# Performance work log

Measured on AMD Instinct MI355X. Metric: run time of the kernel, lower is better.

The kernel has to match this reference:

```python
import jax, jax.numpy as jnp
import numpy as np

S, B, I, H = 512, 128, 256, 512  # seq_len, batch, input_size, hidden_size


def setup_inputs() -> dict:
    key = jax.random.key(0)
    ks = jax.random.split(key, 5)
    # Gates stacked in order (f, i, o, c), each Linear init'd like nn.Linear
    lim_w = 1.0 / np.sqrt(I)
    lim_u = 1.0 / np.sqrt(H)
    x = jax.random.normal(ks[0], (S, B, I), dtype=jnp.float32)
    W = jax.random.uniform(ks[1], (4 * H, I), minval=-lim_w, maxval=lim_w, dtype=jnp.float32)
    bW = jax.random.uniform(ks[2], (4 * H,), minval=-lim_w, maxval=lim_w, dtype=jnp.float32)
    U = jax.random.uniform(ks[3], (4 * H, H), minval=-lim_u, maxval=lim_u, dtype=jnp.float32)
    bU = jax.random.uniform(ks[4], (4 * H,), minval=-lim_u, maxval=lim_u, dtype=jnp.float32)
    return {"x": x, "W": W, "bW": bW, "U": U, "bU": bU}


def reference(x, W, bW, U, bU):
    """LSTM over time-major x. Gates stacked (f, i, o, c) along dim 0 of W/U.
    Returns (h_seq [S,B,H], h_final [B,H], c_final [B,H]).
    The original's bf/bi/bo/bc buffers are zeros and thus omitted."""
    Hh = U.shape[1]
    # Input projection for all timesteps + both Linear biases, done once.
    xg = jnp.einsum('sbi,gi->sbg', x, W) + bW + bU  # [S, B, 4H]

    def step(carry, xg_t):
        h, c = carry
        g = xg_t + h @ U.T  # [B, 4H]
        f = jax.nn.sigmoid(g[:, 0 * Hh:1 * Hh])
        i = jax.nn.sigmoid(g[:, 1 * Hh:2 * Hh])
        o = jax.nn.sigmoid(g[:, 2 * Hh:3 * Hh])
        cand = jnp.tanh(g[:, 3 * Hh:4 * Hh])
        c_new = f * c + i * cand
        h_new = o * jnp.tanh(c_new)
        return (h_new, c_new), h_new

    b = x.shape[1]
    init = (jnp.zeros((b, Hh), x.dtype), jnp.zeros((b, Hh), x.dtype))
    (h_fin, c_fin), h_seq = jax.lax.scan(step, init, xg)
    return h_seq, h_fin, c_fin
```

## Files before the change

### kernel.cpp

```cpp
#include <hip/hip_runtime.h>
#include <hip/hip_bf16.h>


#define S_LEN 512
#define BATCH 128
#define ISZ   256
#define HSZ   512

typedef __attribute__((ext_vector_type(8))) short  s16x8;
typedef __attribute__((ext_vector_type(4))) float  f32x4;

#define FLAG_BYTES 4096
#define HOFF   4096
#define HBYTES ((size_t)2 * BATCH * HSZ * 2)
#define XOFF   (HOFF + HBYTES)
#define XBYTES ((size_t)S_LEN * BATCH * ISZ * 2)
#define WS_NEED (XOFF + XBYTES)

__device__ __forceinline__ unsigned short f2bf(float f) {
    unsigned u = __float_as_uint(f);
    u += 0x7fffu + ((u >> 16) & 1u);
    return (unsigned short)(u >> 16);
}

__device__ __forceinline__ s16x8 ld8f_bf(const float* p) {
    f32x4 a = *(const f32x4*)p;
    f32x4 b = *(const f32x4*)(p + 4);
    s16x8 r;
    r[0] = (short)f2bf(a[0]); r[1] = (short)f2bf(a[1]);
    r[2] = (short)f2bf(a[2]); r[3] = (short)f2bf(a[3]);
    r[4] = (short)f2bf(b[0]); r[5] = (short)f2bf(b[1]);
    r[6] = (short)f2bf(b[2]); r[7] = (short)f2bf(b[3]);
    return r;
}

__global__ void __launch_bounds__(256, 1)
cvt_x_kernel(const float* __restrict__ x, unsigned short* __restrict__ xbf, int n8) {
    int i = blockIdx.x * blockDim.x + threadIdx.x;
    const int stride = gridDim.x * blockDim.x;
    for (; i < n8; i += stride)
        *(s16x8*)(xbf + (size_t)i * 8) = ld8f_bf(x + (size_t)i * 8);
}

#define MFMA_BF16 __builtin_amdgcn_mfma_f32_16x16x32_bf16

template <bool BIGWS>
__global__ void __launch_bounds__(256, 1)
lstm_kq3(const float* __restrict__ x,
         const float* __restrict__ W,
         const float* __restrict__ bW,
         const float* __restrict__ U,
         const float* __restrict__ bU,
         float* __restrict__ out,
         unsigned char* __restrict__ ws)
{
    __shared__ float g_lds[2][4][16][68];

    const int tid  = threadIdx.x;
    const int bid  = blockIdx.x;
    const int grp  = bid & 7;
    const int wg   = bid >> 3;
    const int jBase = wg * 16;
    const int rBase = grp * 16;

    unsigned* flags = (unsigned*)ws;
    unsigned short* h0 = (unsigned short*)(ws + HOFF);
    unsigned short* h1 = h0 + BATCH * HSZ;
    const unsigned short* xbf = (const unsigned short*)(ws + XOFF);

    const int kq   = tid >> 6;
    const int lane = tid & 63;
    const int l15  = lane & 15;
    const int lq   = lane >> 4;
    const int arow = rBase + l15;

    s16x8 ub[4][4], wb[4][2];
    float bias[4];
    #pragma unroll
    for (int n = 0; n < 4; ++n) {
        const int gRow = n * HSZ + jBase + l15;
        bias[n] = (kq == 0) ? (bW[gRow] + bU[gRow]) : 0.f;
        #pragma unroll
        for (int ki = 0; ki < 4; ++ki)
            ub[n][ki] = ld8f_bf(U + (size_t)gRow * HSZ + kq * 128 + ki * 32 + lq * 8);
        #pragma unroll
        for (int ki = 0; ki < 2; ++ki)
            wb[n][ki] = ld8f_bf(W + (size_t)gRow * ISZ + kq * 64 + ki * 32 + lq * 8);
    }

    const int er = tid >> 4, ej = tid & 15;
    const int orow = rBase + er, ocol = jBase + ej;
    float cst = 0.f;

    for (int t = 0; t < S_LEN; ++t) {
        const int par = t & 1;
        f32x4 acc[4] = { { bias[0], bias[0], bias[0], bias[0] },
                         { bias[1], bias[1], bias[1], bias[1] },
                         { bias[2], bias[2], bias[2], bias[2] },
                         { bias[3], bias[3], bias[3], bias[3] } };

        #pragma unroll
        for (int ki = 0; ki < 2; ++ki) {
            s16x8 a;
            if constexpr (BIGWS)
                a = *(const s16x8*)(xbf + ((size_t)t * BATCH + arow) * ISZ
                                    + kq * 64 + ki * 32 + lq * 8);
            else
                a = ld8f_bf(x + ((size_t)t * BATCH + arow) * ISZ
                            + kq * 64 + ki * 32 + lq * 8);
            #pragma unroll
            for (int n = 0; n < 4; ++n)
                acc[n] = MFMA_BF16(a, wb[n][ki], acc[n], 0, 0, 0);
        }

        if (t > 0) {
            const unsigned* fp = flags + grp * 128 + kq * 32 + (lane & 31);
            const unsigned tgt = (unsigned)t;
            for (;;) {
                unsigned v;
                asm volatile("global_load_dword %0, %1, off sc0 sc1\n\t"
                             "s_waitcnt vmcnt(0)"
                             : "=&v"(v) : "v"(fp) : "memory");
                if (__all(v >= tgt)) break;
            }
            __builtin_amdgcn_sched_barrier(0);

            const unsigned short* hp = (par ? h0 : h1)
                                       + (size_t)arow * HSZ + kq * 128 + lq * 8;
            s16x8 f0, f1, f2, f3;
#define LDH(d, o) asm volatile("global_load_dwordx4 %0, %1, off offset:" o " sc0 sc1" \
                               : "=&v"(d) : "v"(hp) : "memory")
            LDH(f0, "0"); LDH(f1, "64"); LDH(f2, "128"); LDH(f3, "192");
#undef LDH
            asm volatile("s_waitcnt vmcnt(2)" ::: "memory");
            __builtin_amdgcn_sched_barrier(0);
            #pragma unroll
            for (int n = 0; n < 4; ++n)
                acc[n] = MFMA_BF16(f0, ub[n][0], acc[n], 0, 0, 0);
            #pragma unroll
            for (int n = 0; n < 4; ++n)
                acc[n] = MFMA_BF16(f1, ub[n][1], acc[n], 0, 0, 0);
            asm volatile("s_waitcnt vmcnt(0)" ::: "memory");
            __builtin_amdgcn_sched_barrier(0);
            #pragma unroll
            for (int n = 0; n < 4; ++n)
                acc[n] = MFMA_BF16(f2, ub[n][2], acc[n], 0, 0, 0);
            #pragma unroll
            for (int n = 0; n < 4; ++n)
                acc[n] = MFMA_BF16(f3, ub[n][3], acc[n], 0, 0, 0);
        }

        #pragma unroll
        for (int n = 0; n < 4; ++n)
            #pragma unroll
            for (int r = 0; r < 4; ++r)
                g_lds[par][kq][lq * 4 + r][n * 16 + l15] = acc[n][r];
        __syncthreads();

        const float gf = g_lds[par][0][er][ej]      + g_lds[par][1][er][ej]
                       + g_lds[par][2][er][ej]      + g_lds[par][3][er][ej];
        const float gi = g_lds[par][0][er][16 + ej] + g_lds[par][1][er][16 + ej]
                       + g_lds[par][2][er][16 + ej] + g_lds[par][3][er][16 + ej];
        const float go = g_lds[par][0][er][32 + ej] + g_lds[par][1][er][32 + ej]
                       + g_lds[par][2][er][32 + ej] + g_lds[par][3][er][32 + ej];
        const float gc = g_lds[par][0][er][48 + ej] + g_lds[par][1][er][48 + ej]
                       + g_lds[par][2][er][48 + ej] + g_lds[par][3][er][48 + ej];

        const float fg = __builtin_amdgcn_rcpf(1.f + __expf(-gf));
        const float ig = __builtin_amdgcn_rcpf(1.f + __expf(-gi));
        const float og = __builtin_amdgcn_rcpf(1.f + __expf(-go));
        const float ec = __expf(-2.f * fabsf(gc));
        const float cd = copysignf((1.f - ec) * __builtin_amdgcn_rcpf(1.f + ec), gc);
        cst = fg * cst + ig * cd;
        const float eh = __expf(-2.f * fabsf(cst));
        const float hn = og * copysignf((1.f - eh) * __builtin_amdgcn_rcpf(1.f + eh), cst);

        if (t < S_LEN - 1) {
            unsigned hv = (unsigned)f2bf(hn);
            unsigned short* hd = (par ? h1 : h0) + (size_t)orow * HSZ + ocol;
            asm volatile("global_store_short %0, %1, off sc0 sc1"
                         :: "v"(hd), "v"(hv) : "memory");
            asm volatile("s_waitcnt vmcnt(0)" ::: "memory");
            if (lane == 0) {
                unsigned* fl = flags + grp * 128 + wg * 4 + kq;
                unsigned ep = (unsigned)(t + 1);
                asm volatile("global_store_dword %0, %1, off sc0 sc1"
                             :: "v"(fl), "v"(ep) : "memory");
            }
            out[((size_t)t * BATCH + orow) * HSZ + ocol] = hn;
        } else {
            out[((size_t)t * BATCH + orow) * HSZ + ocol] = hn;
            const size_t HSEQ = (size_t)S_LEN * BATCH * HSZ;
            out[HSEQ + (size_t)orow * HSZ + ocol] = hn;
            out[HSEQ + (size_t)BATCH * HSZ + (size_t)orow * HSZ + ocol] = cst;
        }
    }
}

extern "C" void kernel_launch(void* const* d_in, const int* in_sizes, int n_in,
                              void* d_out, int out_size, void* d_ws, size_t ws_size,
                              hipStream_t stream) {
    const float* x  = (const float*)d_in[0];
    const float* W  = (const float*)d_in[1];
    const float* bW = (const float*)d_in[2];
    const float* U  = (const float*)d_in[3];
    const float* bU = (const float*)d_in[4];
    float* out = (float*)d_out;
    unsigned char* ws = (unsigned char*)d_ws;

    hipMemsetAsync(ws, 0, FLAG_BYTES, stream);

    void* args[] = { (void*)&x, (void*)&W, (void*)&bW, (void*)&U, (void*)&bU,
                     (void*)&out, (void*)&ws };

    if (ws_size >= WS_NEED) {
        const int n8 = S_LEN * BATCH * ISZ / 8;
        cvt_x_kernel<<<2048, 256, 0, stream>>>(x, (unsigned short*)(ws + XOFF), n8);
        hipError_t e = hipLaunchCooperativeKernel((void*)lstm_kq3<true>, dim3(256),
                                                  dim3(256), args, 0, stream);
        if (e != hipSuccess)
            lstm_kq3<true><<<dim3(256), dim3(256), 0, stream>>>(x, W, bW, U, bU, out, ws);
    } else {
        hipError_t e = hipLaunchCooperativeKernel((void*)lstm_kq3<false>, dim3(256),
                                                  dim3(256), args, 0, stream);
        if (e != hipSuccess)
            lstm_kq3<false><<<dim3(256), dim3(256), 0, stream>>>(x, W, bW, U, bU, out, ws);
    }
}
```

Baseline: 1.292 ms.

## Triple-buffer hidden state and pipeline flag polling with two outstanding loads

The hidden-state exchange buffer grows from two slots to three, rotated via wslot/rslot, so a fast block writing step t+1 cannot overwrite data a slow block is still reading. The spin-wait on per-group flags now keeps two flag loads in flight and checks them alternately, which shortens each polling round trip. The cost is extra workspace and more outstanding memory traffic while spinning. The point of the third slot is to keep correctness safe under the relaxed overlap.

```diff
diff --git a/kernel.cpp b/kernel.cpp
--- a/kernel.cpp
+++ b/kernel.cpp
@@ -12,7 +12,7 @@
 
 #define FLAG_BYTES 4096
 #define HOFF   4096
-#define HBYTES ((size_t)2 * BATCH * HSZ * 2)
+#define HBYTES ((size_t)3 * BATCH * HSZ * 2)
 #define XOFF   (HOFF + HBYTES)
 #define XBYTES ((size_t)S_LEN * BATCH * ISZ * 2)
 #define WS_NEED (XOFF + XBYTES)
@@ -46,7 +46,7 @@
 
 template <bool BIGWS>
 __global__ void __launch_bounds__(256, 1)
-lstm_kq3(const float* __restrict__ x,
+lstm_kq5(const float* __restrict__ x,
          const float* __restrict__ W,
          const float* __restrict__ bW,
          const float* __restrict__ U,
@@ -64,8 +64,7 @@
     const int rBase = grp * 16;
 
     unsigned* flags = (unsigned*)ws;
-    unsigned short* h0 = (unsigned short*)(ws + HOFF);
-    unsigned short* h1 = h0 + BATCH * HSZ;
+    unsigned short* hb = (unsigned short*)(ws + HOFF);
     const unsigned short* xbf = (const unsigned short*)(ws + XOFF);
 
     const int kq   = tid >> 6;
@@ -91,6 +90,8 @@
     const int er = tid >> 4, ej = tid & 15;
     const int orow = rBase + er, ocol = jBase + ej;
     float cst = 0.f;
+
+    int wslot = 0, rslot = 2;
 
     for (int t = 0; t < S_LEN; ++t) {
         const int par = t & 1;
@@ -116,16 +117,25 @@
         if (t > 0) {
             const unsigned* fp = flags + grp * 128 + kq * 32 + (lane & 31);
             const unsigned tgt = (unsigned)t;
+            unsigned vA, vB;
+            asm volatile("global_load_dword %0, %1, off sc0 sc1"
+                         : "=&v"(vA) : "v"(fp) : "memory");
+            asm volatile("global_load_dword %0, %1, off sc0 sc1"
+                         : "=&v"(vB) : "v"(fp) : "memory");
             for (;;) {
-                unsigned v;
-                asm volatile("global_load_dword %0, %1, off sc0 sc1\n\t"
-                             "s_waitcnt vmcnt(0)"
-                             : "=&v"(v) : "v"(fp) : "memory");
-                if (__all(v >= tgt)) break;
+                asm volatile("s_waitcnt vmcnt(1)" ::: "memory");
+                __builtin_amdgcn_sched_barrier(0);
+                if (__all(vA >= tgt)) break;
+                asm volatile("global_load_dword %0, %1, off sc0 sc1"
+                             : "=&v"(vA) : "v"(fp) : "memory");
+                asm volatile("s_waitcnt vmcnt(1)" ::: "memory");
+                __builtin_amdgcn_sched_barrier(0);
+                if (__all(vB >= tgt)) break;
+                asm volatile("global_load_dword %0, %1, off sc0 sc1"
+                             : "=&v"(vB) : "v"(fp) : "memory");
             }
-            __builtin_amdgcn_sched_barrier(0);
-
-            const unsigned short* hp = (par ? h0 : h1)
+
+            const unsigned short* hp = hb + (rslot << 16)
                                        + (size_t)arow * HSZ + kq * 128 + lq * 8;
             s16x8 f0, f1, f2, f3;
 #define LDH(d, o) asm volatile("global_load_dwordx4 %0, %1, off offset:" o " sc0 sc1" \
@@ -134,6 +144,7 @@
 #undef LDH
             asm volatile("s_waitcnt vmcnt(2)" ::: "memory");
             __builtin_amdgcn_sched_barrier(0);
+            asm volatile("" :: "v"(vA), "v"(vB));
             #pragma unroll
             for (int n = 0; n < 4; ++n)
                 acc[n] = MFMA_BF16(f0, ub[n][0], acc[n], 0, 0, 0);
@@ -177,7 +188,7 @@
 
         if (t < S_LEN - 1) {
             unsigned hv = (unsigned)f2bf(hn);
-            unsigned short* hd = (par ? h1 : h0) + (size_t)orow * HSZ + ocol;
+            unsigned short* hd = hb + (wslot << 16) + (size_t)orow * HSZ + ocol;
             asm volatile("global_store_short %0, %1, off sc0 sc1"
                          :: "v"(hd), "v"(hv) : "memory");
             asm volatile("s_waitcnt vmcnt(0)" ::: "memory");
@@ -194,6 +205,9 @@
             out[HSEQ + (size_t)orow * HSZ + ocol] = hn;
             out[HSEQ + (size_t)BATCH * HSZ + (size_t)orow * HSZ + ocol] = cst;
         }
+
+        rslot = wslot;
+        wslot = (wslot == 2) ? 0 : wslot + 1;
     }
 }
 
@@ -216,14 +230,14 @@
     if (ws_size >= WS_NEED) {
         const int n8 = S_LEN * BATCH * ISZ / 8;
         cvt_x_kernel<<<2048, 256, 0, stream>>>(x, (unsigned short*)(ws + XOFF), n8);
-        hipError_t e = hipLaunchCooperativeKernel((void*)lstm_kq3<true>, dim3(256),
+        hipError_t e = hipLaunchCooperativeKernel((void*)lstm_kq5<true>, dim3(256),
                                                   dim3(256), args, 0, stream);
         if (e != hipSuccess)
-            lstm_kq3<true><<<dim3(256), dim3(256), 0, stream>>>(x, W, bW, U, bU, out, ws);
+            lstm_kq5<true><<<dim3(256), dim3(256), 0, stream>>>(x, W, bW, U, bU, out, ws);
     } else {
-        hipError_t e = hipLaunchCooperativeKernel((void*)lstm_kq3<false>, dim3(256),
+        hipError_t e = hipLaunchCooperativeKernel((void*)lstm_kq5<false>, dim3(256),
                                                   dim3(256), args, 0, stream);
         if (e != hipSuccess)
-            lstm_kq3<false><<<dim3(256), dim3(256), 0, stream>>>(x, W, bW, U, bU, out, ws);
+            lstm_kq5<false><<<dim3(256), dim3(256), 0, stream>>>(x, W, bW, U, bU, out, ws);
     }
 }
```

Result: no change. 1.282 ms, median of 2 (-0.8%).
